# Performance work log

Measured on AMD Instinct MI355X. Metric: run time of the kernel, lower is better.

The kernel has to match this reference:

```python
import jax, jax.numpy as jnp
import numpy as np

N_NODES = 100000
N_EDGES = 1200000
D = 64
N_REL = 2
N_BASIS = 16
N_LAYERS = 3  # num_layer=2 -> 3 stacked CompGCNLayer stages


def setup_inputs() -> dict:
    key = jax.random.key(0)
    ks = jax.random.split(key, 12)
    s = 1.0 / np.sqrt(D)
    return {
        "h_u": jax.random.normal(ks[0], (N_NODES, D), jnp.float32),
        "Basis": jax.random.normal(ks[1], (N_BASIS, D), jnp.float32) * (1.0 / np.sqrt(N_BASIS)),
        "alpha": jax.random.normal(ks[2], (N_REL + 1, N_BASIS), jnp.float32),
        "W_O": jax.random.normal(ks[3], (N_LAYERS, D, D), jnp.float32) * s,
        "W_I": jax.random.normal(ks[4], (N_LAYERS, D, D), jnp.float32) * s,
        "W_S": jax.random.normal(ks[5], (N_LAYERS, D, D), jnp.float32) * s,
        "W_rel": jax.random.normal(ks[6], (N_LAYERS, D, D), jnp.float32) * s,
        "src": jax.random.randint(ks[7], (N_EDGES,), 0, N_NODES, jnp.int32),
        "dst": jax.random.randint(ks[8], (N_EDGES,), 0, N_NODES, jnp.int32),
        "edge_etype": jax.random.randint(ks[9], (N_EDGES,), 0, N_REL, jnp.int32),
        "edge_dir": jax.random.randint(ks[10], (N_EDGES,), 0, 2, jnp.int32),  # 0=out, 1=in
    }


def reference(h_u, Basis, alpha, W_O, W_I, W_S, W_rel, src, dst, edge_etype, edge_dir):
    # relation representations: rows 0..N_REL-1 are etypes, row N_REL is self_loop
    h_r = alpha @ Basis  # [N_REL+1, D]
    is_in = (edge_dir == 1)[:, None]  # [E,1]

    for l in range(N_LAYERS):
        # composition 'sub': comp_m = h_src - h_edge_rel
        comp_m = h_u[src] - h_r[edge_etype]               # [E, D]
        # per-direction linear transform (Linear: x @ W.T)
        m_out = comp_m @ W_O[l].T
        m_in = comp_m @ W_I[l].T
        msg = jnp.where(is_in, m_in, m_out)               # [E, D]
        # scatter-sum aggregation (copy_e + sum)
        agg = jax.ops.segment_sum(msg, dst, num_segments=N_NODES)  # [N, D]
        # self-loop branch
        comp_s = h_u - h_r[-1]                            # [N, D]
        h_v = comp_s @ W_S[l].T + agg
        h_r = h_r @ W_rel[l].T
        if l < N_LAYERS - 1:  # last layer has act=None
            h_v = jax.nn.relu(h_v)
            h_r = jax.nn.relu(h_r)
        h_u = h_v
    return h_u
```

## Files before the change

kernel.cpp:

```cpp
#include <hip/hip_runtime.h>

constexpr int D = 64;
constexpr int NREL = 2;
constexpr int NBASIS = 16;
constexpr int NLAYERS = 3;
constexpr int SCAN_CHUNK = 1024;
constexpr int BSH = 9;
constexpr int BNODES = 1 << BSH;
constexpr int PB = 256;
constexpr int TR = 32;

__global__ void hr_init_kernel(const float* __restrict__ alpha,
                               const float* __restrict__ basis,
                               float* __restrict__ hr) {
  int t = threadIdx.x;
  int r = t >> 6, d = t & 63;
  float s = 0.f;
  for (int b = 0; b < NBASIS; ++b) s += alpha[r * NBASIS + b] * basis[b * D + d];
  hr[r * D + d] = s;
}

__global__ void hr_update_kernel(const float* __restrict__ hr_in,
                                 const float* __restrict__ Wrel,
                                 float* __restrict__ hr_out, int do_relu) {
  int t = threadIdx.x;
  int r = t >> 6, d = t & 63;
  float s = 0.f;
  for (int k = 0; k < D; ++k) s += hr_in[r * D + k] * Wrel[d * D + k];
  if (do_relu) s = fmaxf(s, 0.f);
  hr_out[r * D + d] = s;
}

__global__ __launch_bounds__(256) void part_hist(const int* __restrict__ dst,
                                                 int* __restrict__ ghist,
                                                 int E, int chunk, int NB) {
  __shared__ int lh[512];
  int blk = blockIdx.x, t = threadIdx.x;
  for (int i = t; i < NB; i += 256) lh[i] = 0;
  __syncthreads();
  int beg = blk * chunk;
  int end = beg + chunk < E ? beg + chunk : E;
  for (int j = beg + t; j < end; j += 256) atomicAdd(&lh[dst[j] >> BSH], 1);
  __syncthreads();
  for (int i = t; i < NB; i += 256) ghist[(size_t)i * PB + blk] = lh[i];
}

__global__ void scan_partial(const int* __restrict__ cnt, int* __restrict__ bsums, int M) {
  int t = threadIdx.x;
  int base = blockIdx.x * SCAN_CHUNK + t * 4;
  int s = 0;
  if (base + 3 < M) {
    int4 v = *(const int4*)(cnt + base);
    s = v.x + v.y + v.z + v.w;
  } else {
    for (int i = 0; i < 4; ++i) if (base + i < M) s += cnt[base + i];
  }
  for (int off = 32; off > 0; off >>= 1) s += __shfl_down(s, off, 64);
  __shared__ int ws[4];
  if ((t & 63) == 0) ws[t >> 6] = s;
  __syncthreads();
  if (t == 0) bsums[blockIdx.x] = ws[0] + ws[1] + ws[2] + ws[3];
}

__global__ void scan_bsums(const int* __restrict__ bsums, int* __restrict__ boffs,
                           int SB, int* __restrict__ totalp) {
  __shared__ int sh[128];
  int t = threadIdx.x;
  int v = (t < SB) ? bsums[t] : 0;
  sh[t] = v;
  __syncthreads();
  for (int off = 1; off < 128; off <<= 1) {
    int u = (t >= off) ? sh[t - off] : 0;
    __syncthreads();
    sh[t] += u;
    __syncthreads();
  }
  if (t < SB) boffs[t] = sh[t] - v;
  if (t == SB - 1) *totalp = sh[t];
}

__global__ void scan_final(const int* __restrict__ cnt, const int* __restrict__ boffs,
                           int* __restrict__ out, int M) {
  int t = threadIdx.x;
  int base = blockIdx.x * SCAN_CHUNK + t * 4;
  int v0 = 0, v1 = 0, v2 = 0, v3 = 0;
  if (base + 3 < M) {
    int4 v = *(const int4*)(cnt + base);
    v0 = v.x; v1 = v.y; v2 = v.z; v3 = v.w;
  } else {
    if (base + 0 < M) v0 = cnt[base + 0];
    if (base + 1 < M) v1 = cnt[base + 1];
    if (base + 2 < M) v2 = cnt[base + 2];
    if (base + 3 < M) v3 = cnt[base + 3];
  }
  int ts = v0 + v1 + v2 + v3;
  int lane = t & 63;
  int incl = ts;
  for (int off = 1; off < 64; off <<= 1) {
    int u = __shfl_up(incl, off, 64);
    if (lane >= off) incl += u;
  }
  __shared__ int wsum[4];
  if (lane == 63) wsum[t >> 6] = incl;
  __syncthreads();
  int woff = 0;
  for (int w = 0; w < (t >> 6); ++w) woff += wsum[w];
  int run = boffs[blockIdx.x] + woff + incl - ts;
  if (base + 0 < M) out[base + 0] = run;
  if (base + 1 < M) out[base + 1] = run + v0;
  if (base + 2 < M) out[base + 2] = run + v0 + v1;
  if (base + 3 < M) out[base + 3] = run + v0 + v1 + v2;
}

__global__ __launch_bounds__(256) void part_scatter(
    const int* __restrict__ src, const int* __restrict__ dst,
    const int* __restrict__ et, const int* __restrict__ dir,
    const int* __restrict__ goffs, int* __restrict__ tmp,
    int E, int chunk, int NB) {
  __shared__ int lc[512];
  int blk = blockIdx.x, t = threadIdx.x;
  for (int i = t; i < NB; i += 256) lc[i] = goffs[(size_t)i * PB + blk];
  __syncthreads();
  int beg = blk * chunk;
  int end = beg + chunk < E ? beg + chunk : E;
  for (int j = beg + t; j < end; j += 256) {
    int d = dst[j];
    int b = d >> BSH;
    int p = atomicAdd(&lc[b], 1);
    tmp[p] = src[j] | (et[j] << 17) | (dir[j] << 18) | ((d & (BNODES - 1)) << 19);
  }
}

__global__ __launch_bounds__(256) void bucket_finalize(
    const int* __restrict__ tmp, const int* __restrict__ goffs,
    int* __restrict__ startv, int* __restrict__ perm, int N, int NB, int E) {
  __shared__ int lcnt[BNODES];
  __shared__ int lstart[BNODES];
  __shared__ int lcur[BNODES];
  __shared__ int spair[256];
  int b = blockIdx.x, t = threadIdx.x;
  int beg = goffs[(size_t)b * PB];
  int end = (b == NB - 1) ? E : goffs[(size_t)(b + 1) * PB];
  lcnt[t] = 0;
  lcnt[t + 256] = 0;
  __syncthreads();
  for (int j = beg + t; j < end; j += 256)
    atomicAdd(&lcnt[(tmp[j] >> 19) & (BNODES - 1)], 1);
  __syncthreads();
  int c0 = lcnt[2 * t], c1 = lcnt[2 * t + 1];
  spair[t] = c0 + c1;
  __syncthreads();
  for (int off = 1; off < 256; off <<= 1) {
    int u = (t >= off) ? spair[t - off] : 0;
    __syncthreads();
    spair[t] += u;
    __syncthreads();
  }
  int epair = spair[t] - (c0 + c1);
  lstart[2 * t] = epair;
  lstart[2 * t + 1] = epair + c0;
  lcur[2 * t] = epair;
  lcur[2 * t + 1] = epair + c0;
  int v0 = (b << BSH) + 2 * t;
  if (v0 < N) startv[v0] = beg + epair;
  if (v0 + 1 < N) startv[v0 + 1] = beg + epair + c0;
  if (b == NB - 1 && t == 0) startv[N] = E;
  __syncthreads();
  for (int j = beg + t; j < end; j += 256) {
    int w = tmp[j];
    int p = atomicAdd(&lcur[(w >> 19) & (BNODES - 1)], 1);
    perm[beg + p] = w & 0x7FFFF;
  }
}

__global__ __launch_bounds__(256) void gather_kernel(
    const float* __restrict__ h, const float* __restrict__ hr,
    const int* __restrict__ start, const int* __restrict__ perm,
    float* __restrict__ aggO, float* __restrict__ aggI, int N) {
  int lane = threadIdx.x & 63;
  int v = blockIdx.x * 4 + (threadIdx.x >> 6);
  if (v >= N) return;
  float hr0 = hr[lane];
  float hr1 = hr[D + lane];
  int beg = start[v], end = start[v + 1];
  float accO = 0.f, accI = 0.f;
  for (int j = beg; j < end; j += 8) {
    int pp[8];
    float ff[8];
#pragma unroll
    for (int u = 0; u < 8; ++u) {
      int jj = j + u < end ? j + u : beg;
      pp[u] = perm[jj];
    }
#pragma unroll
    for (int u = 0; u < 8; ++u)
      ff[u] = h[(size_t)(pp[u] & 0x1FFFF) * D + lane];
#pragma unroll
    for (int u = 0; u < 8; ++u) {
      if (j + u < end) {
        float c = ff[u] - (((pp[u] >> 17) & 1) ? hr1 : hr0);
        if (pp[u] & (1 << 18)) accI += c; else accO += c;
      }
    }
  }
  aggO[(size_t)v * D + lane] = accO;
  aggI[(size_t)v * D + lane] = accI;
}

__global__ __launch_bounds__(256, 2) void node_kernel(
    const float* __restrict__ h_in, const float* __restrict__ aggO,
    const float* __restrict__ aggI, const float* __restrict__ WS,
    const float* __restrict__ WO, const float* __restrict__ WI,
    const float* __restrict__ hr_self, float* __restrict__ h_out,
    int do_relu, int N, int ntiles) {
  __shared__ float4 lws[64 * 17];
  __shared__ float4 lwo[64 * 17];
  __shared__ float4 lwi[64 * 17];
  __shared__ float4 xs[3][TR * 16];
  int tid = threadIdx.x;
  const float4* gws = (const float4*)WS;
  const float4* gwo = (const float4*)WO;
  const float4* gwi = (const float4*)WI;
  for (int i = tid; i < 1024; i += 256) {
    int dd = i >> 4, k4 = i & 15;
    lws[dd * 17 + k4] = gws[i];
    lwo[dd * 17 + k4] = gwo[i];
    lwi[dd * 17 + k4] = gwi[i];
  }
  int lane = tid & 63;
  int wv = tid >> 6;
  const float4* hr4 = (const float4*)hr_self;

  for (int tile = blockIdx.x; tile < ntiles; tile += gridDim.x) {
    int row0 = tile * TR;
    __syncthreads();
    for (int i = tid; i < TR * 16; i += 256) {
      int r = i >> 4, k4 = i & 15;
      int row = row0 + r;
      if (row < N) {
        size_t base = (size_t)row * 16 + k4;
        float4 xh = ((const float4*)h_in)[base];
        float4 hs = hr4[k4];
        xh.x -= hs.x; xh.y -= hs.y; xh.z -= hs.z; xh.w -= hs.w;
        xs[0][i] = xh;
        xs[1][i] = ((const float4*)aggO)[base];
        xs[2][i] = ((const float4*)aggI)[base];
      }
    }
    __syncthreads();
    float acc[8];
#pragma unroll
    for (int r = 0; r < 8; ++r) acc[r] = 0.f;
    for (int k4 = 0; k4 < 16; ++k4) {
      float4 ws4 = lws[lane * 17 + k4];
      float4 wo4 = lwo[lane * 17 + k4];
      float4 wi4 = lwi[lane * 17 + k4];
#pragma unroll
      for (int r = 0; r < 8; ++r) {
        int lr = (wv * 8 + r) * 16 + k4;
        float4 xh = xs[0][lr];
        float4 xo = xs[1][lr];
        float4 xi = xs[2][lr];
        acc[r] += xh.x * ws4.x + xh.y * ws4.y + xh.z * ws4.z + xh.w * ws4.w +
                  xo.x * wo4.x + xo.y * wo4.y + xo.z * wo4.z + xo.w * wo4.w +
                  xi.x * wi4.x + xi.y * wi4.y + xi.z * wi4.z + xi.w * wi4.w;
      }
    }
#pragma unroll
    for (int r = 0; r < 8; ++r) {
      int row = row0 + wv * 8 + r;
      if (row < N) {
        float v = acc[r];
        if (do_relu) v = fmaxf(v, 0.f);
        h_out[(size_t)row * D + lane] = v;
      }
    }
  }
}

extern "C" void kernel_launch(void* const* d_in, const int* in_sizes, int n_in,
                              void* d_out, int out_size, void* d_ws, size_t ws_size,
                              hipStream_t stream) {
  const float* h_u   = (const float*)d_in[0];
  const float* Basis = (const float*)d_in[1];
  const float* alpha = (const float*)d_in[2];
  const float* W_O   = (const float*)d_in[3];
  const float* W_I   = (const float*)d_in[4];
  const float* W_S   = (const float*)d_in[5];
  const float* W_rel = (const float*)d_in[6];
  const int* src  = (const int*)d_in[7];
  const int* dst  = (const int*)d_in[8];
  const int* et   = (const int*)d_in[9];
  const int* edir = (const int*)d_in[10];
  int N = in_sizes[0] / D;
  int E = in_sizes[7];
  int NB = (N + BNODES - 1) >> BSH;
  int M = NB * PB;
  int chunk = (E + PB - 1) / PB;

  char* ws = (char*)d_ws;
  size_t off = 0;
  auto alloc = [&](size_t bytes) -> void* {
    void* p = ws + off;
    off = (off + bytes + 255) & ~(size_t)255;
    return p;
  };
  float* h_buf = (float*)alloc((size_t)N * D * 4);
  float* aggO  = (float*)alloc((size_t)N * D * 4);
  float* aggI  = (float*)alloc((size_t)N * D * 4);
  float* hrA   = (float*)alloc(192 * 4);
  float* hrB   = (float*)alloc(192 * 4);
  int* startv  = (int*)alloc((size_t)(N + 1) * 4);
  int* perm    = (int*)alloc((size_t)E * 4);
  int* tmp     = (int*)alloc((size_t)E * 4);
  int* ghist   = (int*)alloc((size_t)M * 4);
  int* goffs   = (int*)alloc((size_t)(M + 1) * 4);
  int SB = (M + SCAN_CHUNK - 1) / SCAN_CHUNK;
  int* bsums   = (int*)alloc((size_t)SB * 4);
  int* boffs   = (int*)alloc((size_t)SB * 4);

  part_hist<<<PB, 256, 0, stream>>>(dst, ghist, E, chunk, NB);
  scan_partial<<<SB, 256, 0, stream>>>(ghist, bsums, M);
  scan_bsums<<<1, 128, 0, stream>>>(bsums, boffs, SB, goffs + M);
  scan_final<<<SB, 256, 0, stream>>>(ghist, boffs, goffs, M);
  part_scatter<<<PB, 256, 0, stream>>>(src, dst, et, edir, goffs, tmp, E, chunk, NB);
  bucket_finalize<<<NB, 256, 0, stream>>>(tmp, goffs, startv, perm, N, NB, E);

  hr_init_kernel<<<1, 192, 0, stream>>>(alpha, Basis, hrA);

  float* hr_cur = hrA;
  float* hr_nxt = hrB;
  int nb_g = (N + 3) / 4;
  int ntiles = (N + TR - 1) / TR;
  int nb_n = ntiles < 1024 ? ntiles : 1024;
  for (int l = 0; l < NLAYERS; ++l) {
    const float* h_src = (l == 0) ? h_u : h_buf;
    gather_kernel<<<nb_g, 256, 0, stream>>>(h_src, hr_cur, startv, perm, aggO, aggI, N);
    float* outp = (l == NLAYERS - 1) ? (float*)d_out : h_buf;
    node_kernel<<<nb_n, 256, 0, stream>>>(
        h_src, aggO, aggI,
        W_S + (size_t)l * D * D, W_O + (size_t)l * D * D, W_I + (size_t)l * D * D,
        hr_cur + 2 * D, outp, (l < NLAYERS - 1) ? 1 : 0, N, ntiles);
    if (l < NLAYERS - 1) {
      hr_update_kernel<<<1, 192, 0, stream>>>(hr_cur, W_rel + (size_t)l * D * D, hr_nxt, 1);
      float* t = hr_cur; hr_cur = hr_nxt; hr_nxt = t;
    }
  }
}
```

Measured before the change: 567.9 us.

## Register-tile node GEMM with 4x4 outputs per thread and precompute all relation reps

Replaces the persistent node kernel, which computed one output column per lane over 8 rows, with a 512-thread block that computes a 4x4 register tile per thread over 128 rows. It stages padded scalar shared-memory tiles and writes float4 outputs. All per-layer relation representations are now computed up front in a single kernel, removing two tiny launches. The new GEMM uses about 150KB of LDS per block, which limits occupancy, and it reloads the weights for every 128-row block.

After: 567.4 us. Within noise of the previous version (-0.1%).

```diff
diff --git a/kernel.cpp b/kernel.cpp
--- a/kernel.cpp
+++ b/kernel.cpp
@@ -1,34 +1,36 @@
 #include <hip/hip_runtime.h>
 
 constexpr int D = 64;
-constexpr int NREL = 2;
 constexpr int NBASIS = 16;
 constexpr int NLAYERS = 3;
 constexpr int SCAN_CHUNK = 1024;
 constexpr int BSH = 9;
 constexpr int BNODES = 1 << BSH;
 constexpr int PB = 256;
-constexpr int TR = 32;
-
-__global__ void hr_init_kernel(const float* __restrict__ alpha,
-                               const float* __restrict__ basis,
-                               float* __restrict__ hr) {
+constexpr int NR = 128;
+
+__global__ void hr_all_kernel(const float* __restrict__ alpha,
+                              const float* __restrict__ basis,
+                              const float* __restrict__ Wrel,
+                              float* __restrict__ hr) {
+  __shared__ float cur[192], nxt[192];
   int t = threadIdx.x;
   int r = t >> 6, d = t & 63;
   float s = 0.f;
   for (int b = 0; b < NBASIS; ++b) s += alpha[r * NBASIS + b] * basis[b * D + d];
-  hr[r * D + d] = s;
-}
-
-__global__ void hr_update_kernel(const float* __restrict__ hr_in,
-                                 const float* __restrict__ Wrel,
-                                 float* __restrict__ hr_out, int do_relu) {
-  int t = threadIdx.x;
-  int r = t >> 6, d = t & 63;
-  float s = 0.f;
-  for (int k = 0; k < D; ++k) s += hr_in[r * D + k] * Wrel[d * D + k];
-  if (do_relu) s = fmaxf(s, 0.f);
-  hr_out[r * D + d] = s;
+  cur[t] = s;
+  hr[t] = s;
+  __syncthreads();
+  for (int l = 0; l < NLAYERS - 1; ++l) {
+    float v = 0.f;
+    for (int k = 0; k < D; ++k) v += cur[r * D + k] * Wrel[l * D * D + d * D + k];
+    v = fmaxf(v, 0.f);
+    nxt[t] = v;
+    hr[(l + 1) * 192 + t] = v;
+    __syncthreads();
+    cur[t] = nxt[t];
+    __syncthreads();
+  }
 }
 
 __global__ __launch_bounds__(256) void part_hist(const int* __restrict__ dst,
@@ -135,7 +137,6 @@
     const int* __restrict__ tmp, const int* __restrict__ goffs,
     int* __restrict__ startv, int* __restrict__ perm, int N, int NB, int E) {
   __shared__ int lcnt[BNODES];
-  __shared__ int lstart[BNODES];
   __shared__ int lcur[BNODES];
   __shared__ int spair[256];
   int b = blockIdx.x, t = threadIdx.x;
@@ -157,8 +158,6 @@
     __syncthreads();
   }
   int epair = spair[t] - (c0 + c1);
-  lstart[2 * t] = epair;
-  lstart[2 * t + 1] = epair + c0;
   lcur[2 * t] = epair;
   lcur[2 * t + 1] = epair + c0;
   int v0 = (b << BSH) + 2 * t;
@@ -207,73 +206,70 @@
   aggI[(size_t)v * D + lane] = accI;
 }
 
-__global__ __launch_bounds__(256, 2) void node_kernel(
+__global__ __launch_bounds__(512) void node_gemm(
     const float* __restrict__ h_in, const float* __restrict__ aggO,
     const float* __restrict__ aggI, const float* __restrict__ WS,
     const float* __restrict__ WO, const float* __restrict__ WI,
     const float* __restrict__ hr_self, float* __restrict__ h_out,
-    int do_relu, int N, int ntiles) {
-  __shared__ float4 lws[64 * 17];
-  __shared__ float4 lwo[64 * 17];
-  __shared__ float4 lwi[64 * 17];
-  __shared__ float4 xs[3][TR * 16];
+    int do_relu, int N) {
+  __shared__ float xh[NR][65], xo[NR][65], xi[NR][65];
+  __shared__ float ws_[64][65], wo_[64][65], wi_[64][65];
   int tid = threadIdx.x;
-  const float4* gws = (const float4*)WS;
-  const float4* gwo = (const float4*)WO;
-  const float4* gwi = (const float4*)WI;
-  for (int i = tid; i < 1024; i += 256) {
-    int dd = i >> 4, k4 = i & 15;
-    lws[dd * 17 + k4] = gws[i];
-    lwo[dd * 17 + k4] = gwo[i];
-    lwi[dd * 17 + k4] = gwi[i];
-  }
-  int lane = tid & 63;
-  int wv = tid >> 6;
+  int row0 = blockIdx.x * NR;
+  for (int idx = tid; idx < 1024; idx += 512) {
+    int d = idx >> 4, k0 = (idx & 15) * 4;
+    float4 a = ((const float4*)WS)[idx];
+    float4 b = ((const float4*)WO)[idx];
+    float4 c = ((const float4*)WI)[idx];
+    ws_[d][k0] = a.x; ws_[d][k0+1] = a.y; ws_[d][k0+2] = a.z; ws_[d][k0+3] = a.w;
+    wo_[d][k0] = b.x; wo_[d][k0+1] = b.y; wo_[d][k0+2] = b.z; wo_[d][k0+3] = b.w;
+    wi_[d][k0] = c.x; wi_[d][k0+1] = c.y; wi_[d][k0+2] = c.z; wi_[d][k0+3] = c.w;
+  }
   const float4* hr4 = (const float4*)hr_self;
-
-  for (int tile = blockIdx.x; tile < ntiles; tile += gridDim.x) {
-    int row0 = tile * TR;
-    __syncthreads();
-    for (int i = tid; i < TR * 16; i += 256) {
-      int r = i >> 4, k4 = i & 15;
-      int row = row0 + r;
-      if (row < N) {
-        size_t base = (size_t)row * 16 + k4;
-        float4 xh = ((const float4*)h_in)[base];
-        float4 hs = hr4[k4];
-        xh.x -= hs.x; xh.y -= hs.y; xh.z -= hs.z; xh.w -= hs.w;
-        xs[0][i] = xh;
-        xs[1][i] = ((const float4*)aggO)[base];
-        xs[2][i] = ((const float4*)aggI)[base];
+  for (int idx = tid; idx < NR * 16; idx += 512) {
+    int r = idx >> 4, kq = idx & 15, k0 = kq * 4;
+    int row = row0 + r;
+    float4 a = make_float4(0.f, 0.f, 0.f, 0.f), b = a, c = a;
+    if (row < N) {
+      size_t g = (size_t)row * 16 + kq;
+      a = ((const float4*)h_in)[g];
+      float4 hs = hr4[kq];
+      a.x -= hs.x; a.y -= hs.y; a.z -= hs.z; a.w -= hs.w;
+      b = ((const float4*)aggO)[g];
+      c = ((const float4*)aggI)[g];
+    }
+    xh[r][k0] = a.x; xh[r][k0+1] = a.y; xh[r][k0+2] = a.z; xh[r][k0+3] = a.w;
+    xo[r][k0] = b.x; xo[r][k0+1] = b.y; xo[r][k0+2] = b.z; xo[r][k0+3] = b.w;
+    xi[r][k0] = c.x; xi[r][k0+1] = c.y; xi[r][k0+2] = c.z; xi[r][k0+3] = c.w;
+  }
+  __syncthreads();
+  int tc4 = (tid & 15) * 4;
+  int tr4 = (tid >> 4) * 4;
+  float acc[4][4] = {{0.f}};
+#define GEMM1(X, W)                                                          \
+  _Pragma("unroll 4")                                                        \
+  for (int k = 0; k < 64; ++k) {                                             \
+    float x0 = X[tr4+0][k], x1 = X[tr4+1][k], x2 = X[tr4+2][k], x3 = X[tr4+3][k]; \
+    float w0 = W[tc4+0][k], w1 = W[tc4+1][k], w2 = W[tc4+2][k], w3 = W[tc4+3][k]; \
+    acc[0][0]+=x0*w0; acc[0][1]+=x0*w1; acc[0][2]+=x0*w2; acc[0][3]+=x0*w3;  \
+    acc[1][0]+=x1*w0; acc[1][1]+=x1*w1; acc[1][2]+=x1*w2; acc[1][3]+=x1*w3;  \
+    acc[2][0]+=x2*w0; acc[2][1]+=x2*w1; acc[2][2]+=x2*w2; acc[2][3]+=x2*w3;  \
+    acc[3][0]+=x3*w0; acc[3][1]+=x3*w1; acc[3][2]+=x3*w2; acc[3][3]+=x3*w3;  \
+  }
+  GEMM1(xh, ws_)
+  GEMM1(xo, wo_)
+  GEMM1(xi, wi_)
+#undef GEMM1
+#pragma unroll
+  for (int i = 0; i < 4; ++i) {
+    int row = row0 + tr4 + i;
+    if (row < N) {
+      float4 o = make_float4(acc[i][0], acc[i][1], acc[i][2], acc[i][3]);
+      if (do_relu) {
+        o.x = fmaxf(o.x, 0.f); o.y = fmaxf(o.y, 0.f);
+        o.z = fmaxf(o.z, 0.f); o.w = fmaxf(o.w, 0.f);
       }
-    }
-    __syncthreads();
-    float acc[8];
-#pragma unroll
-    for (int r = 0; r < 8; ++r) acc[r] = 0.f;
-    for (int k4 = 0; k4 < 16; ++k4) {
-      float4 ws4 = lws[lane * 17 + k4];
-      float4 wo4 = lwo[lane * 17 + k4];
-      float4 wi4 = lwi[lane * 17 + k4];
-#pragma unroll
-      for (int r = 0; r < 8; ++r) {
-        int lr = (wv * 8 + r) * 16 + k4;
-        float4 xh = xs[0][lr];
-        float4 xo = xs[1][lr];
-        float4 xi = xs[2][lr];
-        acc[r] += xh.x * ws4.x + xh.y * ws4.y + xh.z * ws4.z + xh.w * ws4.w +
-                  xo.x * wo4.x + xo.y * wo4.y + xo.z * wo4.z + xo.w * wo4.w +
-                  xi.x * wi4.x + xi.y * wi4.y + xi.z * wi4.z + xi.w * wi4.w;
-      }
-    }
-#pragma unroll
-    for (int r = 0; r < 8; ++r) {
-      int row = row0 + wv * 8 + r;
-      if (row < N) {
-        float v = acc[r];
-        if (do_relu) v = fmaxf(v, 0.f);
-        h_out[(size_t)row * D + lane] = v;
-      }
+      ((float4*)h_out)[(size_t)row * 16 + (tc4 >> 2)] = o;
     }
   }
 }
@@ -308,8 +304,7 @@
   float* h_buf = (float*)alloc((size_t)N * D * 4);
   float* aggO  = (float*)alloc((size_t)N * D * 4);
   float* aggI  = (float*)alloc((size_t)N * D * 4);
-  float* hrA   = (float*)alloc(192 * 4);
-  float* hrB   = (float*)alloc(192 * 4);
+  float* hrbuf = (float*)alloc(3 * 192 * 4);
   int* startv  = (int*)alloc((size_t)(N + 1) * 4);
   int* perm    = (int*)alloc((size_t)E * 4);
   int* tmp     = (int*)alloc((size_t)E * 4);
@@ -326,24 +321,18 @@
   part_scatter<<<PB, 256, 0, stream>>>(src, dst, et, edir, goffs, tmp, E, chunk, NB);
   bucket_finalize<<<NB, 256, 0, stream>>>(tmp, goffs, startv, perm, N, NB, E);
 
-  hr_init_kernel<<<1, 192, 0, stream>>>(alpha, Basis, hrA);
-
-  float* hr_cur = hrA;
-  float* hr_nxt = hrB;
+  hr_all_kernel<<<1, 192, 0, stream>>>(alpha, Basis, W_rel, hrbuf);
+
   int nb_g = (N + 3) / 4;
-  int ntiles = (N + TR - 1) / TR;
-  int nb_n = ntiles < 1024 ? ntiles : 1024;
+  int nb_n = (N + NR - 1) / NR;
   for (int l = 0; l < NLAYERS; ++l) {
     const float* h_src = (l == 0) ? h_u : h_buf;
-    gather_kernel<<<nb_g, 256, 0, stream>>>(h_src, hr_cur, startv, perm, aggO, aggI, N);
+    const float* hr_l = hrbuf + l * 192;
+    gather_kernel<<<nb_g, 256, 0, stream>>>(h_src, hr_l, startv, perm, aggO, aggI, N);
     float* outp = (l == NLAYERS - 1) ? (float*)d_out : h_buf;
-    node_kernel<<<nb_n, 256, 0, stream>>>(
+    node_gemm<<<nb_n, 512, 0, stream>>>(
         h_src, aggO, aggI,
         W_S + (size_t)l * D * D, W_O + (size_t)l * D * D, W_I + (size_t)l * D * D,
-        hr_cur + 2 * D, outp, (l < NLAYERS - 1) ? 1 : 0, N, ntiles);
-    if (l < NLAYERS - 1) {
-      hr_update_kernel<<<1, 192, 0, stream>>>(hr_cur, W_rel + (size_t)l * D * D, hr_nxt, 1);
-      float* t = hr_cur; hr_cur = hr_nxt; hr_nxt = t;
-    }
-  }
-}
+        hr_l + 2 * D, outp, (l < NLAYERS - 1) ? 1 : 0, N);
+  }
+}
```
